# Kernel tuning notes

Measured on AMD Instinct MI355X. Metric: run time of the kernel, lower is better.

Reference implementation:

```python
import jax, jax.numpy as jnp
import numpy as np

B, T, I, H, O = 64, 2048, 256, 256, 128

def _rnn_scan(xp, W_hh):
    # xp: [T, B, H] = precomputed W_ih @ x + b_ih + b_hh per timestep
    h0 = jnp.zeros((xp.shape[1], W_hh.shape[0]), xp.dtype)
    def step(h, xt):
        h_new = jnp.tanh(xt + h @ W_hh.T)
        return h_new, h_new
    _, hs = jax.lax.scan(step, h0, xp)
    return hs  # [T, B, H]

def setup_inputs() -> dict:
    key = jax.random.key(0)
    ks = jax.random.split(key, 9)
    s1 = 1.0 / np.sqrt(H)
    s2 = 1.0 / np.sqrt(O)
    return {
        "x": jax.random.normal(ks[0], (B, T, I), dtype=jnp.float32),
        "W_ih1": jax.random.normal(ks[1], (H, I), dtype=jnp.float32) * s1,
        "W_hh1": jax.random.normal(ks[2], (H, H), dtype=jnp.float32) * s1,
        "b_ih1": jax.random.normal(ks[3], (H,), dtype=jnp.float32) * s1,
        "b_hh1": jax.random.normal(ks[4], (H,), dtype=jnp.float32) * s1,
        "W_ih2": jax.random.normal(ks[5], (O, H), dtype=jnp.float32) * s2,
        "W_hh2": jax.random.normal(ks[6], (O, O), dtype=jnp.float32) * s2,
        "b_ih2": jax.random.normal(ks[7], (O,), dtype=jnp.float32) * s2,
        "b_hh2": jax.random.normal(ks[8], (O,), dtype=jnp.float32) * s2,
    }

def reference(x, W_ih1, W_hh1, b_ih1, b_hh1, W_ih2, W_hh2, b_ih2, b_hh2):
    # Layer 1: h_t = tanh(W_ih1 x_t + b_ih1 + W_hh1 h_{t-1} + b_hh1)
    xp1 = jnp.einsum('bti,hi->tbh', x, W_ih1) + (b_ih1 + b_hh1)
    h1 = _rnn_scan(xp1, W_hh1)                      # [T, B, H]
    # Layer 2: o_t = tanh(W_ih2 h_t + b_ih2 + W_hh2 o_{t-1} + b_hh2)
    xp2 = jnp.einsum('tbh,oh->tbo', h1, W_ih2) + (b_ih2 + b_hh2)
    h2 = _rnn_scan(xp2, W_hh2)                      # [T, B, O]
    out = jnp.transpose(h2, (1, 0, 2)).reshape(-1, O)  # [B*T, num_classes]
    return out
```

## Files before the change

### kernel.cpp

```cpp
#include <hip/hip_runtime.h>
#include <math.h>

#define BB 64
#define TT 2048
#define II 256
#define HH 256
#define OO 128

template<int N>
__global__ __launch_bounds__(256)
void gemm_bias(const float* __restrict__ A, const float* __restrict__ W,
               const float* __restrict__ b1, const float* __restrict__ b2,
               float* __restrict__ C)
{
    constexpr int K = 256;
    __shared__ float sA[16][132];
    __shared__ float sB[16][132];
    const int tid  = threadIdx.x;
    const long row0 = (long)blockIdx.x * 128;
    const int  col0 = blockIdx.y * 128;

    const int tm = tid & 15;
    const int tn = tid >> 4;

    float acc[8][8];
#pragma unroll
    for (int i = 0; i < 8; ++i)
#pragma unroll
        for (int j = 0; j < 8; ++j) acc[i][j] = 0.f;

    const int f0  = tid;
    const int f1  = tid + 256;
    const int am0 = f0 >> 2, ak0 = (f0 & 3) * 4;
    const int am1 = f1 >> 2, ak1 = (f1 & 3) * 4;

    for (int kt = 0; kt < K; kt += 16) {
        float4 a0 = *(const float4*)&A[(row0 + am0) * K + kt + ak0];
        float4 a1 = *(const float4*)&A[(row0 + am1) * K + kt + ak1];
        float4 w0 = *(const float4*)&W[(long)(col0 + am0) * K + kt + ak0];
        float4 w1 = *(const float4*)&W[(long)(col0 + am1) * K + kt + ak1];
        __syncthreads();
        sA[ak0+0][am0] = a0.x; sA[ak0+1][am0] = a0.y; sA[ak0+2][am0] = a0.z; sA[ak0+3][am0] = a0.w;
        sA[ak1+0][am1] = a1.x; sA[ak1+1][am1] = a1.y; sA[ak1+2][am1] = a1.z; sA[ak1+3][am1] = a1.w;
        sB[ak0+0][am0] = w0.x; sB[ak0+1][am0] = w0.y; sB[ak0+2][am0] = w0.z; sB[ak0+3][am0] = w0.w;
        sB[ak1+0][am1] = w1.x; sB[ak1+1][am1] = w1.y; sB[ak1+2][am1] = w1.z; sB[ak1+3][am1] = w1.w;
        __syncthreads();
#pragma unroll
        for (int k = 0; k < 16; ++k) {
            float4 av0 = *(const float4*)&sA[k][tm * 8];
            float4 av1 = *(const float4*)&sA[k][tm * 8 + 4];
            float4 bv0 = *(const float4*)&sB[k][tn * 8];
            float4 bv1 = *(const float4*)&sB[k][tn * 8 + 4];
            float am[8] = {av0.x, av0.y, av0.z, av0.w, av1.x, av1.y, av1.z, av1.w};
            float bn[8] = {bv0.x, bv0.y, bv0.z, bv0.w, bv1.x, bv1.y, bv1.z, bv1.w};
#pragma unroll
            for (int i = 0; i < 8; ++i)
#pragma unroll
                for (int j = 0; j < 8; ++j)
                    acc[i][j] += am[i] * bn[j];
        }
    }

    float bias[8];
#pragma unroll
    for (int j = 0; j < 8; ++j) {
        int col = col0 + tn * 8 + j;
        bias[j] = b1[col] + b2[col];
    }
#pragma unroll
    for (int i = 0; i < 8; ++i) {
        long row = row0 + tm * 8 + i;
        float4 v0, v1;
        v0.x = acc[i][0] + bias[0]; v0.y = acc[i][1] + bias[1];
        v0.z = acc[i][2] + bias[2]; v0.w = acc[i][3] + bias[3];
        v1.x = acc[i][4] + bias[4]; v1.y = acc[i][5] + bias[5];
        v1.z = acc[i][6] + bias[6]; v1.w = acc[i][7] + bias[7];
        *(float4*)&C[row * N + col0 + tn * 8]     = v0;
        *(float4*)&C[row * N + col0 + tn * 8 + 4] = v1;
    }
}

__device__ __forceinline__ float fast_tanh(float x) {
    float e = __expf(2.f * x);
    return 1.f - 2.f / (e + 1.f);
}

__global__ __launch_bounds__(512, 2)
void rnn_pipe(const float* __restrict__ W_hh1,
              const float* __restrict__ W_ih2,
              const float* __restrict__ W_hh2,
              const float* __restrict__ b_ih2,
              const float* __restrict__ b_hh2,
              float* __restrict__ XH,
              float* __restrict__ out,
              int* __restrict__ flags)
{
    const int tid = threadIdx.x;
    const int g   = tid & 31;
    const int ks  = tid >> 5;

    if (blockIdx.x < BB) {
        __shared__ float h_lds[256];
        __shared__ float part[16 * 256];
        const int b = blockIdx.x;

        float4 w[8][4];
#pragma unroll
        for (int r = 0; r < 8; ++r)
#pragma unroll
            for (int c = 0; c < 4; ++c)
                w[r][c] = *(const float4*)&W_hh1[(g * 8 + r) * 256 + ks * 16 + c * 4];

        float* rowp = XH + (long)b * TT * HH;
        float xp = 0.f;
        if (tid < 256) {
            h_lds[tid] = 0.f;
            xp = rowp[tid];
        }
        __syncthreads();

        for (int t = 0; t < TT; ++t) {
            float4 h4[4];
#pragma unroll
            for (int c = 0; c < 4; ++c)
                h4[c] = *(const float4*)&h_lds[ks * 16 + c * 4];

            float acc[8];
#pragma unroll
            for (int r = 0; r < 8; ++r) acc[r] = 0.f;
#pragma unroll
            for (int c = 0; c < 4; ++c)
#pragma unroll
                for (int r = 0; r < 8; ++r)
                    acc[r] += w[r][c].x * h4[c].x + w[r][c].y * h4[c].y
                            + w[r][c].z * h4[c].z + w[r][c].w * h4[c].w;

            *(float4*)&part[ks * 256 + g * 8]     = make_float4(acc[0], acc[1], acc[2], acc[3]);
            *(float4*)&part[ks * 256 + g * 8 + 4] = make_float4(acc[4], acc[5], acc[6], acc[7]);
            __syncthreads();

            if (tid < 256) {
                float s0 = part[0 * 256 + tid] + part[1 * 256 + tid]
                         + part[2 * 256 + tid] + part[3 * 256 + tid];
                float s1 = part[4 * 256 + tid] + part[5 * 256 + tid]
                         + part[6 * 256 + tid] + part[7 * 256 + tid];
                float s2 = part[8 * 256 + tid] + part[9 * 256 + tid]
                         + part[10 * 256 + tid] + part[11 * 256 + tid];
                float s3 = part[12 * 256 + tid] + part[13 * 256 + tid]
                         + part[14 * 256 + tid] + part[15 * 256 + tid];
                float v = fast_tanh(((s0 + s1) + (s2 + s3)) + xp);
                h_lds[tid] = v;
                rowp[(long)t * HH + tid] = v;
                if (t + 1 < TT) xp = rowp[(long)(t + 1) * HH + tid];
            }
            __syncthreads();

            if ((t & 3) == 3 && tid == 0)
                __hip_atomic_store(&flags[b], t + 1, __ATOMIC_RELEASE,
                                   __HIP_MEMORY_SCOPE_AGENT);
        }
    } else {
        __shared__ float h1_lds[256];
        __shared__ float o_lds[128];
        __shared__ float part2[16 * 132];
        const int b = blockIdx.x - BB;

        float4 wi[4][4];
        float4 wh[4][2];
#pragma unroll
        for (int r = 0; r < 4; ++r) {
#pragma unroll
            for (int c = 0; c < 4; ++c)
                wi[r][c] = *(const float4*)&W_ih2[(g * 4 + r) * 256 + ks * 16 + c * 4];
#pragma unroll
            for (int c = 0; c < 2; ++c)
                wh[r][c] = *(const float4*)&W_hh2[(g * 4 + r) * 128 + ks * 8 + c * 4];
        }

        float bias = 0.f;
        if (tid < 128) {
            bias = b_ih2[tid] + b_hh2[tid];
            o_lds[tid] = 0.f;
        }
        const float* h1p = XH + (long)b * TT * HH;
        float* outp      = out + (long)b * TT * OO;
        __syncthreads();

        int seen = 0;
        for (int t = 0; t < TT; ++t) {
            if (seen <= t) {
                do {
                    seen = __hip_atomic_load(&flags[b], __ATOMIC_ACQUIRE,
                                             __HIP_MEMORY_SCOPE_AGENT);
                } while (seen <= t);
            }
            if (tid < 64)
                *(float4*)&h1_lds[tid * 4] = *(const float4*)&h1p[(long)t * HH + tid * 4];
            __syncthreads();

            float4 h4[4];
#pragma unroll
            for (int c = 0; c < 4; ++c)
                h4[c] = *(const float4*)&h1_lds[ks * 16 + c * 4];
            float4 o4[2];
#pragma unroll
            for (int c = 0; c < 2; ++c)
                o4[c] = *(const float4*)&o_lds[ks * 8 + c * 4];

            float acc[4];
#pragma unroll
            for (int r = 0; r < 4; ++r) acc[r] = 0.f;
#pragma unroll
            for (int c = 0; c < 4; ++c)
#pragma unroll
                for (int r = 0; r < 4; ++r)
                    acc[r] += wi[r][c].x * h4[c].x + wi[r][c].y * h4[c].y
                            + wi[r][c].z * h4[c].z + wi[r][c].w * h4[c].w;
#pragma unroll
            for (int c = 0; c < 2; ++c)
#pragma unroll
                for (int r = 0; r < 4; ++r)
                    acc[r] += wh[r][c].x * o4[c].x + wh[r][c].y * o4[c].y
                            + wh[r][c].z * o4[c].z + wh[r][c].w * o4[c].w;

            *(float4*)&part2[ks * 132 + g * 4] = make_float4(acc[0], acc[1], acc[2], acc[3]);
            __syncthreads();

            if (tid < 128) {
                float s = bias;
#pragma unroll
                for (int s16 = 0; s16 < 16; ++s16)
                    s += part2[s16 * 132 + tid];
                float v = fast_tanh(s);
                o_lds[tid] = v;
                outp[(long)t * OO + tid] = v;
            }
        }
    }
}

extern "C" void kernel_launch(void* const* d_in, const int* in_sizes, int n_in,
                              void* d_out, int out_size, void* d_ws, size_t ws_size,
                              hipStream_t stream)
{
    const float* x     = (const float*)d_in[0];
    const float* W_ih1 = (const float*)d_in[1];
    const float* W_hh1 = (const float*)d_in[2];
    const float* b_ih1 = (const float*)d_in[3];
    const float* b_hh1 = (const float*)d_in[4];
    const float* W_ih2 = (const float*)d_in[5];
    const float* W_hh2 = (const float*)d_in[6];
    const float* b_ih2 = (const float*)d_in[7];
    const float* b_hh2 = (const float*)d_in[8];
    float* out = (float*)d_out;

    float* xp1 = (float*)d_ws;
    const size_t FLAG_OFF = (size_t)BB * TT * HH * sizeof(float);
    int* flags = (int*)((char*)d_ws + FLAG_OFF);

    const int M = BB * TT;

    hipMemsetAsync(flags, 0, BB * sizeof(int), stream);

    dim3 gA(M / 128, HH / 128);
    gemm_bias<HH><<<gA, 256, 0, stream>>>(x, W_ih1, b_ih1, b_hh1, xp1);

    rnn_pipe<<<2 * BB, 512, 0, stream>>>(W_hh1, W_ih2, W_hh2, b_ih2, b_hh2,
                                         xp1, out, flags);
}
```

Before: 2.084 ms.

## Restructure layer-1 partial-sum layout, single-thread flag polling, relax launch bounds

The layer-1 partial-sum store now writes two float4 halves at stride 128, and the reduction reads through a permuted index. This is meant to reduce LDS bank conflicts on the float4 writes. The layer-2 consumer now has only thread 0 spin on the flag with relaxed loads, follow with one acquire load, and broadcast the value through shared memory and a barrier, instead of every thread spinning with acquire semantics. The launch-bounds occupancy hint of 2 is dropped, so the compiler has more registers for the weights held in registers, at the cost of an extra barrier per wait.

```diff
diff --git a/kernel.cpp b/kernel.cpp
--- a/kernel.cpp
+++ b/kernel.cpp
@@ -85,7 +85,7 @@
     return 1.f - 2.f / (e + 1.f);
 }
 
-__global__ __launch_bounds__(512, 2)
+__global__ __launch_bounds__(512)
 void rnn_pipe(const float* __restrict__ W_hh1,
               const float* __restrict__ W_ih2,
               const float* __restrict__ W_hh2,
@@ -117,6 +117,7 @@
             h_lds[tid] = 0.f;
             xp = rowp[tid];
         }
+        const int ro = ((tid & 7) >> 2) * 128 + ((tid >> 3) << 2) + (tid & 3);
         __syncthreads();
 
         for (int t = 0; t < TT; ++t) {
@@ -135,19 +136,19 @@
                     acc[r] += w[r][c].x * h4[c].x + w[r][c].y * h4[c].y
                             + w[r][c].z * h4[c].z + w[r][c].w * h4[c].w;
 
-            *(float4*)&part[ks * 256 + g * 8]     = make_float4(acc[0], acc[1], acc[2], acc[3]);
-            *(float4*)&part[ks * 256 + g * 8 + 4] = make_float4(acc[4], acc[5], acc[6], acc[7]);
+            *(float4*)&part[ks * 256 + g * 4]       = make_float4(acc[0], acc[1], acc[2], acc[3]);
+            *(float4*)&part[ks * 256 + 128 + g * 4] = make_float4(acc[4], acc[5], acc[6], acc[7]);
             __syncthreads();
 
             if (tid < 256) {
-                float s0 = part[0 * 256 + tid] + part[1 * 256 + tid]
-                         + part[2 * 256 + tid] + part[3 * 256 + tid];
-                float s1 = part[4 * 256 + tid] + part[5 * 256 + tid]
-                         + part[6 * 256 + tid] + part[7 * 256 + tid];
-                float s2 = part[8 * 256 + tid] + part[9 * 256 + tid]
-                         + part[10 * 256 + tid] + part[11 * 256 + tid];
-                float s3 = part[12 * 256 + tid] + part[13 * 256 + tid]
-                         + part[14 * 256 + tid] + part[15 * 256 + tid];
+                float s0 = part[0 * 256 + ro] + part[1 * 256 + ro]
+                         + part[2 * 256 + ro] + part[3 * 256 + ro];
+                float s1 = part[4 * 256 + ro] + part[5 * 256 + ro]
+                         + part[6 * 256 + ro] + part[7 * 256 + ro];
+                float s2 = part[8 * 256 + ro] + part[9 * 256 + ro]
+                         + part[10 * 256 + ro] + part[11 * 256 + ro];
+                float s3 = part[12 * 256 + ro] + part[13 * 256 + ro]
+                         + part[14 * 256 + ro] + part[15 * 256 + ro];
                 float v = fast_tanh(((s0 + s1) + (s2 + s3)) + xp);
                 h_lds[tid] = v;
                 rowp[(long)t * HH + tid] = v;
@@ -163,6 +164,7 @@
         __shared__ float h1_lds[256];
         __shared__ float o_lds[128];
         __shared__ float part2[16 * 132];
+        __shared__ int   seen_sh;
         const int b = blockIdx.x - BB;
 
         float4 wi[4][4];
@@ -189,10 +191,18 @@
         int seen = 0;
         for (int t = 0; t < TT; ++t) {
             if (seen <= t) {
-                do {
-                    seen = __hip_atomic_load(&flags[b], __ATOMIC_ACQUIRE,
-                                             __HIP_MEMORY_SCOPE_AGENT);
-                } while (seen <= t);
+                if (tid == 0) {
+                    int s;
+                    do {
+                        s = __hip_atomic_load(&flags[b], __ATOMIC_RELAXED,
+                                              __HIP_MEMORY_SCOPE_AGENT);
+                    } while (s <= t);
+                    s = __hip_atomic_load(&flags[b], __ATOMIC_ACQUIRE,
+                                          __HIP_MEMORY_SCOPE_AGENT);
+                    seen_sh = s;
+                }
+                __syncthreads();
+                seen = seen_sh;
             }
             if (tid < 64)
                 *(float4*)&h1_lds[tid * 4] = *(const float4*)&h1p[(long)t * HH + tid * 4];
@@ -260,7 +270,7 @@
 
     const int M = BB * TT;
 
-    hipMemsetAsync(flags, 0, BB * sizeof(int), stream);
+    (void)hipMemsetAsync(flags, 0, BB * sizeof(int), stream);
 
     dim3 gA(M / 128, HH / 128);
     gemm_bias<HH><<<gA, 256, 0, stream>>>(x, W_ih1, b_ih1, b_hh1, xp1);
```

After: 2.018 ms. 3.1% less time.
